# Optimization experiments

Measured on AMD Instinct MI355X. Metric: run time of the kernel, lower is better.

The kernel has to match this reference:

```python
import jax, jax.numpy as jnp
import numpy as np

DIM = 1024
HEADS = 16
HEAD_DIM = DIM // HEADS
HIDDEN = int(DIM * 4.0)
EPS = 1e-5


def setup_inputs() -> dict:
    key = jax.random.key(0)
    ks = jax.random.split(key, 16)
    s = 0.02
    inp = {
        'x': jax.random.normal(ks[0], (2, 2048, DIM), dtype=jnp.float32),
        'g1': jnp.ones((DIM,), jnp.float32),
        'b1': jnp.zeros((DIM,), jnp.float32),
        'Wq': jax.random.normal(ks[1], (DIM, DIM)) * s,
        'bq': jnp.zeros((DIM,), jnp.float32),
        'Wk': jax.random.normal(ks[2], (DIM, DIM)) * s,
        'bk': jnp.zeros((DIM,), jnp.float32),
        'Wv': jax.random.normal(ks[3], (DIM, DIM)) * s,
        'bv': jnp.zeros((DIM,), jnp.float32),
        'Wo': jax.random.normal(ks[4], (DIM, DIM)) * s,
        'bo': jnp.zeros((DIM,), jnp.float32),
        'g2': jnp.ones((DIM,), jnp.float32),
        'b2': jnp.zeros((DIM,), jnp.float32),
        'W1': jax.random.normal(ks[5], (DIM, HIDDEN)) * s,
        'bf1': jnp.zeros((HIDDEN,), jnp.float32),
        'W2': jax.random.normal(ks[6], (HIDDEN, DIM)) * s,
        'bf2': jnp.zeros((DIM,), jnp.float32),
    }
    return inp


def _layernorm(x, g, b):
    mu = jnp.mean(x, axis=-1, keepdims=True)
    var = jnp.mean((x - mu) ** 2, axis=-1, keepdims=True)
    return (x - mu) * jax.lax.rsqrt(var + EPS) * g + b


def _block(x, g1, b1, Wq, bq, Wk, bk, Wv, bv, Wo, bo, g2, b2, W1, bf1, W2, bf2):
    B, N, C = x.shape
    h = _layernorm(x, g1, b1)
    # project and split heads: [B, H, N, D]
    q = (h @ Wq + bq).reshape(B, N, HEADS, HEAD_DIM).transpose(0, 2, 1, 3)
    k = (h @ Wk + bk).reshape(B, N, HEADS, HEAD_DIM).transpose(0, 2, 1, 3)
    v = (h @ Wv + bv).reshape(B, N, HEADS, HEAD_DIM).transpose(0, 2, 1, 3)
    scale = HEAD_DIM ** -0.5
    attn = jnp.einsum('bhqd,bhkd->bhqk', q, k) * scale
    attn = jax.nn.softmax(attn, axis=-1)
    o = jnp.einsum('bhqk,bhkd->bhqd', attn, v)
    o = o.transpose(0, 2, 1, 3).reshape(B, N, C)
    x = x + (o @ Wo + bo)
    h = _layernorm(x, g2, b2)
    h = jax.nn.gelu(h @ W1 + bf1, approximate=False)
    x = x + (h @ W2 + bf2)
    return x


def reference(x, g1, b1, Wq, bq, Wk, bk, Wv, bv, Wo, bo, g2, b2, W1, bf1, W2, bf2):
    return _block(x, g1, b1, Wq, bq, Wk, bk, Wv, bv, Wo, bo, g2, b2, W1, bf1, W2, bf2)
```

## Files before the change

### kernel.cpp

```cpp
#include <hip/hip_runtime.h>
#include <hip/hip_bf16.h>
#include <math.h>


typedef unsigned short ushort_t;
typedef short short8 __attribute__((ext_vector_type(8)));
typedef float f32x4 __attribute__((ext_vector_type(4)));

#define TOKENS 4096
#define SEQ    2048
#define DIMC   1024
#define HID    4096

__device__ __forceinline__ float bf2f(ushort_t u) {
    union { float f; unsigned int u; } c; c.u = ((unsigned int)u) << 16; return c.f;
}
__device__ __forceinline__ ushort_t f2bf(float f) {
    union { float f; unsigned int u; } c; c.f = f;
    unsigned int u = c.u;
    unsigned int r = u + 0x7fffu + ((u >> 16) & 1u);
    return (ushort_t)(r >> 16);
}
__device__ __forceinline__ float gelu_f(float x) {
    const float y = 0.79788456080286536f * (x + 0.044715f * x * x * x);
    const float t = __expf(-2.0f * fabsf(y));
    const float th = (1.0f - t) / (1.0f + t);
    return 0.5f * x * (1.0f + copysignf(th, y));
}
__device__ __forceinline__ float load_elem(const void* p, size_t i, int isbf) {
    return isbf ? bf2f(((const ushort_t*)p)[i]) : ((const float*)p)[i];
}

__global__ __launch_bounds__(256) void detect_dtype(
    const ushort_t* __restrict__ x, int* __restrict__ flag)
{
    __shared__ int bad;
    if (threadIdx.x == 0) bad = 0;
    __syncthreads();
    for (int i = threadIdx.x; i < 4096; i += 256) {
        float v = bf2f(x[i]);
        if (!(fabsf(v) <= 1e6f)) bad = 1;
    }
    __syncthreads();
    if (threadIdx.x == 0) { flag[0] = (bad == 0) ? 1 : 0; flag[1] = 1; }
}

__global__ __launch_bounds__(256) void transpose_w_all(
    const void* __restrict__ Wq, const void* __restrict__ Wk,
    const void* __restrict__ Wv, const void* __restrict__ Wo,
    const void* __restrict__ W1, const void* __restrict__ W2,
    ushort_t* __restrict__ wsq, ushort_t* __restrict__ w1t,
    ushort_t* __restrict__ w2t, const int* __restrict__ flag)
{
    __shared__ ushort_t tile[32][33];
    const int isbf = *flag;
    const int id = blockIdx.x;
    const void* in; ushort_t* out; int K, N, bx, by;
    if (id < 4096) {
        const int z = id >> 10, t = id & 1023;
        in = z == 0 ? Wq : (z == 1 ? Wk : (z == 2 ? Wv : Wo));
        out = wsq + (size_t)z * DIMC * DIMC;
        K = DIMC; N = DIMC; bx = t & 31; by = t >> 5;
    } else if (id < 8192) {
        const int t = id - 4096;
        in = W1; out = w1t; K = DIMC; N = HID;
        bx = t & 127; by = t >> 7;
    } else {
        const int t = id - 8192;
        in = W2; out = w2t; K = HID; N = DIMC;
        bx = t & 31; by = t >> 5;
    }
    const int kb = by * 32, nb = bx * 32;
    const int tx = threadIdx.x & 31, ty = threadIdx.x >> 5;
    for (int i = 0; i < 4; i++) {
        int k = kb + ty + i * 8;
        tile[ty + i * 8][tx] = f2bf(load_elem(in, (size_t)k * N + nb + tx, isbf));
    }
    __syncthreads();
    for (int i = 0; i < 4; i++) {
        int n = nb + ty + i * 8;
        out[(size_t)n * K + kb + tx] = tile[tx][ty + i * 8];
    }
}

template<int INMODE>
__global__ __launch_bounds__(256) void ln_kernel(
    const void* __restrict__ in, const void* __restrict__ g,
    const void* __restrict__ b, const int* __restrict__ flag,
    ushort_t* __restrict__ out)
{
    const int isbf = *flag;
    const int t = blockIdx.x;
    const int tid = threadIdx.x;
    const size_t base = (size_t)t * DIMC;
    float v[4];
    for (int i = 0; i < 4; i++) {
        int idx = tid + i * 256;
        v[i] = (INMODE == 1) ? ((const float*)in)[base + idx]
                             : load_elem(in, base + idx, isbf);
    }
    float s  = v[0] + v[1] + v[2] + v[3];
    float s2 = v[0]*v[0] + v[1]*v[1] + v[2]*v[2] + v[3]*v[3];
    for (int off = 1; off < 64; off <<= 1) {
        s  += __shfl_xor(s,  off);
        s2 += __shfl_xor(s2, off);
    }
    __shared__ float red[8];
    const int wave = tid >> 6, lane = tid & 63;
    if (lane == 0) { red[wave] = s; red[wave + 4] = s2; }
    __syncthreads();
    s  = red[0] + red[1] + red[2] + red[3];
    s2 = red[4] + red[5] + red[6] + red[7];
    const float mu  = s * (1.0f / DIMC);
    const float var = s2 * (1.0f / DIMC) - mu * mu;
    const float inv = rsqrtf(fmaxf(var, 0.f) + 1e-5f);
    for (int i = 0; i < 4; i++) {
        int idx = tid + i * 256;
        float o = (v[i] - mu) * inv * load_elem(g, idx, isbf) + load_elem(b, idx, isbf);
        out[base + idx] = f2bf(o);
    }
}

template<int BN, int RES, int ACT, int OUTF>
__global__ __launch_bounds__(256) void gemm_bt(
    const ushort_t* __restrict__ A, const ushort_t* __restrict__ BT,
    const void* __restrict__ bias0, const void* __restrict__ bias1,
    const void* __restrict__ bias2, const void* __restrict__ resid,
    void* __restrict__ out0, void* __restrict__ out1, void* __restrict__ out2,
    int M, int N, int K, int Ksub, const int* __restrict__ flag)
{
    constexpr int BM   = 128;
    constexpr int JF   = BN / 32;
    constexpr int ASEG = BM / 16;
    constexpr int SPW  = (BM + BN) / 64;
    __shared__ __align__(16) ushort_t As[BM][32];
    __shared__ __align__(16) ushort_t Bs[BN][32];
    const int isbf = *flag;
    const int tid = threadIdx.x, lane = tid & 63, wave = tid >> 6;
    const int m0 = blockIdx.y * BM, n0 = blockIdx.x * BN;
    const int wm = (wave & 1) * 64;
    const int wn = (wave >> 1) * (BN / 2);
    const int lm = lane & 15, quad = lane >> 4;

    const void* biasp = bias0;
    void* outp = out0;
    int nout = N;
    int colmask = 0x7fffffff;
    int sel = 0;
    if (OUTF == 3) {
        sel = n0 >> 10;
        biasp = sel == 0 ? bias0 : (sel == 1 ? bias1 : bias2);
        outp  = sel == 0 ? out0  : (sel == 1 ? out1  : out2);
        nout = 1024; colmask = 1023;
    }
    int kbeg = 0;
    if (OUTF == 4) {
        kbeg = blockIdx.z * Ksub;
        outp = blockIdx.z ? out1 : out0;
    }

    f32x4 acc[4][JF];
    for (int i = 0; i < 4; i++)
        for (int j = 0; j < JF; j++)
            acc[i][j] = (f32x4){0.f, 0.f, 0.f, 0.f};

    const int lrow = lane >> 2;
    const int lcol = (lane & 3) * 8;

    for (int k0 = kbeg; k0 < kbeg + Ksub; k0 += 32) {
#pragma unroll
        for (int s = 0; s < SPW; s++) {
            const int seg = wave * SPW + s;
            const ushort_t* gp;
            ushort_t* lp;
            if (seg < ASEG) {
                gp = &A[(size_t)(m0 + seg * 16 + lrow) * K + k0 + lcol];
                lp = &As[seg * 16][0];
            } else {
                gp = &BT[(size_t)(n0 + (seg - ASEG) * 16 + lrow) * K + k0 + lcol];
                lp = &Bs[(seg - ASEG) * 16][0];
            }
            __builtin_amdgcn_global_load_lds(
                (const __attribute__((address_space(1))) unsigned int*)gp,
                (__attribute__((address_space(3))) unsigned int*)lp, 16, 0, 0);
        }
        __syncthreads();
        short8 af[4], bfr[JF];
#pragma unroll
        for (int i = 0; i < 4; i++) af[i] = *(const short8*)&As[wm + i * 16 + lm][quad * 8];
#pragma unroll
        for (int j = 0; j < JF; j++) bfr[j] = *(const short8*)&Bs[wn + j * 16 + lm][quad * 8];
#pragma unroll
        for (int i = 0; i < 4; i++)
#pragma unroll
            for (int j = 0; j < JF; j++)
                acc[i][j] = __builtin_amdgcn_mfma_f32_16x16x32_bf16(af[i], bfr[j], acc[i][j], 0, 0, 0);
        __syncthreads();
    }

    if (OUTF == 3 && sel == 2) {
        for (int j = 0; j < JF; j++) {
            const int colo = (n0 + wn + j * 16 + lm) & 1023;
            const float bv = load_elem(biasp, colo, isbf);
            for (int i = 0; i < 4; i++) {
                const int token = m0 + wm + i * 16 + quad * 4;
                const int bb = token >> 11, ss = token & 2047;
                unsigned int lo = (unsigned int)f2bf(acc[i][j][0] + bv)
                                | ((unsigned int)f2bf(acc[i][j][1] + bv) << 16);
                unsigned int hi = (unsigned int)f2bf(acc[i][j][2] + bv)
                                | ((unsigned int)f2bf(acc[i][j][3] + bv) << 16);
                *(uint2*)&((ushort_t*)outp)[(size_t)((bb << 10) + colo) * SEQ + ss] =
                    make_uint2(lo, hi);
            }
        }
        return;
    }

    for (int j = 0; j < JF; j++) {
        const int col  = n0 + wn + j * 16 + lm;
        const int colo = col & colmask;
        const float bv = (OUTF == 4) ? 0.f : load_elem(biasp, colo, isbf);
        for (int i = 0; i < 4; i++) {
            const int rbase = m0 + wm + i * 16 + quad * 4;
            for (int r = 0; r < 4; r++) {
                const size_t oi = (size_t)(rbase + r) * nout + colo;
                float v2 = acc[i][j][r] + bv;
                if (ACT == 1) v2 = gelu_f(v2);
                if (RES == 1) v2 += load_elem(resid, oi, isbf);
                if (RES == 2) v2 += ((const float*)resid)[oi];
                if (OUTF == 1 || OUTF == 4) { ((float*)outp)[oi] = v2; }
                else if (OUTF == 2) {
                    if (isbf) ((ushort_t*)outp)[oi] = f2bf(v2);
                    else      ((float*)outp)[oi] = v2;
                }
                else                { ((ushort_t*)outp)[oi] = f2bf(v2); }
            }
        }
    }
}

template<int RESRAW, int OUTF32>
__global__ __launch_bounds__(256) void splitk_reduce(
    const float* __restrict__ p0, const float* __restrict__ p1,
    const void* __restrict__ bias, const void* __restrict__ resid,
    void* __restrict__ out, const int* __restrict__ flag)
{
    const int isbf = *flag;
    const size_t i = ((size_t)blockIdx.x * 256 + threadIdx.x) * 4;
    const float4 a = *(const float4*)&p0[i];
    const float4 b = *(const float4*)&p1[i];
    const int col = (int)(i & 1023);
    float v[4] = {a.x + b.x, a.y + b.y, a.z + b.z, a.w + b.w};
    for (int c = 0; c < 4; c++) {
        v[c] += load_elem(bias, col + c, isbf);
        v[c] += RESRAW ? load_elem(resid, i + c, isbf) : ((const float*)resid)[i + c];
    }
    if (OUTF32) {
        *(float4*)&((float*)out)[i] = make_float4(v[0], v[1], v[2], v[3]);
    } else if (isbf) {
        unsigned int lo = (unsigned int)f2bf(v[0]) | ((unsigned int)f2bf(v[1]) << 16);
        unsigned int hi = (unsigned int)f2bf(v[2]) | ((unsigned int)f2bf(v[3]) << 16);
        *(uint2*)&((ushort_t*)out)[i] = make_uint2(lo, hi);
    } else {
        *(float4*)&((float*)out)[i] = make_float4(v[0], v[1], v[2], v[3]);
    }
}

__global__ __launch_bounds__(256) void attn_kernel(
    const ushort_t* __restrict__ q, const ushort_t* __restrict__ k,
    const ushort_t* __restrict__ vt, ushort_t* __restrict__ o)
{
    const int bh = blockIdx.x;
    const int b  = bh >> 4, h = bh & 15;
    const int q0 = blockIdx.y * 128;
    const int tid = threadIdx.x, lane = tid & 63, wave = tid >> 6;
    const int lm = lane & 15, quad = lane >> 4;

    __shared__ ushort_t Qs[128][72];
    __shared__ ushort_t Ks[64][72];
    __shared__ ushort_t Vt[64][72];
    __shared__ ushort_t Ps[4][32][72];

    const size_t base  = ((size_t)b * SEQ) * DIMC + h * 64;
    const size_t vbase = ((size_t)b * DIMC + h * 64) * SEQ;

    {
        const int er0 = (tid * 8) >> 6;
        const int ec0 = (tid * 8) & 63;
        for (int half = 0; half < 4; half++) {
            const int r = er0 + half * 32;
            short8 qq = *(const short8*)&q[base + (size_t)(q0 + r) * DIMC + ec0];
            short8 qs;
            for (int i = 0; i < 8; i++)
                qs[i] = (short)f2bf(bf2f((ushort_t)qq[i]) * 0.18033688011112042f);
            *(short8*)&Qs[r][ec0] = qs;
        }
    }
    __syncthreads();

    short8 qf[2][2];
    for (int qh = 0; qh < 2; qh++)
        for (int ks = 0; ks < 2; ks++)
            qf[qh][ks] = *(const short8*)&Qs[wave * 32 + qh * 16 + lm][quad * 8 + ks * 32];

    short8 onef;
    for (int i = 0; i < 8; i++) onef[i] = (short)0x3F80;

    f32x4 oacc[4][2], lacc[2];
    for (int j = 0; j < 4; j++)
        for (int qh = 0; qh < 2; qh++) oacc[j][qh] = (f32x4){0.f, 0.f, 0.f, 0.f};
    lacc[0] = (f32x4){0.f, 0.f, 0.f, 0.f};
    lacc[1] = (f32x4){0.f, 0.f, 0.f, 0.f};

    const int er = (tid * 8) >> 6;
    const int ec = (tid * 8) & 63;
    const int dd = tid >> 2;
    const int kg = tid & 3;

    short8 kreg0, kreg1, vreg0, vreg1;
    {
        kreg0 = *(const short8*)&k[base + (size_t)(er) * DIMC + ec];
        kreg1 = *(const short8*)&k[base + (size_t)(er + 32) * DIMC + ec];
        const size_t vsrc = vbase + (size_t)dd * SEQ + kg * 16;
        vreg0 = *(const short8*)&vt[vsrc];
        vreg1 = *(const short8*)&vt[vsrc + 8];
    }

    for (int kt = 0; kt < SEQ / 64; kt++) {
        __syncthreads();
        *(short8*)&Ks[er][ec]          = kreg0;
        *(short8*)&Ks[er + 32][ec]     = kreg1;
        *(short8*)&Vt[dd][kg * 16]     = vreg0;
        *(short8*)&Vt[dd][kg * 16 + 8] = vreg1;
        __syncthreads();
        if (kt + 1 < SEQ / 64) {
            const int kn = (kt + 1) * 64;
            kreg0 = *(const short8*)&k[base + (size_t)(kn + er) * DIMC + ec];
            kreg1 = *(const short8*)&k[base + (size_t)(kn + er + 32) * DIMC + ec];
            const size_t vsrc = vbase + (size_t)dd * SEQ + kn + kg * 16;
            vreg0 = *(const short8*)&vt[vsrc];
            vreg1 = *(const short8*)&vt[vsrc + 8];
        }

        f32x4 st[4][2];
        for (int j = 0; j < 4; j++)
            for (int qh = 0; qh < 2; qh++) st[j][qh] = (f32x4){0.f, 0.f, 0.f, 0.f};
        for (int ks = 0; ks < 2; ks++) {
            for (int j = 0; j < 4; j++) {
                short8 kf = *(const short8*)&Ks[j * 16 + lm][quad * 8 + ks * 32];
                for (int qh = 0; qh < 2; qh++)
                    st[j][qh] = __builtin_amdgcn_mfma_f32_16x16x32_bf16(kf, qf[qh][ks], st[j][qh], 0, 0, 0);
            }
        }

        for (int j = 0; j < 4; j++)
            for (int qh = 0; qh < 2; qh++) {
                unsigned int u0 = __float_as_uint(__builtin_amdgcn_exp2f(st[j][qh][0]));
                unsigned int u1 = __float_as_uint(__builtin_amdgcn_exp2f(st[j][qh][1]));
                unsigned int u2 = __float_as_uint(__builtin_amdgcn_exp2f(st[j][qh][2]));
                unsigned int u3 = __float_as_uint(__builtin_amdgcn_exp2f(st[j][qh][3]));
                unsigned int lo = (u1 & 0xffff0000u) | (u0 >> 16);
                unsigned int hi = (u3 & 0xffff0000u) | (u2 >> 16);
                *(uint2*)&Ps[wave][qh * 16 + lm][j * 16 + quad * 4] = make_uint2(lo, hi);
            }

        for (int ks = 0; ks < 2; ks++) {
            for (int qh = 0; qh < 2; qh++) {
                short8 pf = *(const short8*)&Ps[wave][qh * 16 + lm][quad * 8 + ks * 32];
                lacc[qh] = __builtin_amdgcn_mfma_f32_16x16x32_bf16(pf, onef, lacc[qh], 0, 0, 0);
                for (int j = 0; j < 4; j++) {
                    short8 vf = *(const short8*)&Vt[j * 16 + lm][quad * 8 + ks * 32];
                    oacc[j][qh] = __builtin_amdgcn_mfma_f32_16x16x32_bf16(pf, vf, oacc[j][qh], 0, 0, 0);
                }
            }
        }
    }

    float rinv[2][4];
    for (int qh = 0; qh < 2; qh++)
        for (int r = 0; r < 4; r++) rinv[qh][r] = 1.0f / fmaxf(lacc[qh][r], 1e-30f);

    for (int j = 0; j < 4; j++)
        for (int qh = 0; qh < 2; qh++)
            for (int r = 0; r < 4; r++) {
                const int row = q0 + wave * 32 + qh * 16 + quad * 4 + r;
                o[base + (size_t)row * DIMC + j * 16 + lm] = f2bf(oacc[j][qh][r] * rinv[qh][r]);
            }
}

extern "C" void kernel_launch(void* const* d_in, const int* in_sizes, int n_in,
                              void* d_out, int out_size, void* d_ws, size_t ws_size,
                              hipStream_t stream)
{
    const void* x   = d_in[0];
    const void* g1  = d_in[1];
    const void* b1  = d_in[2];
    const void* Wq  = d_in[3];
    const void* bq  = d_in[4];
    const void* Wk  = d_in[5];
    const void* bk  = d_in[6];
    const void* Wv  = d_in[7];
    const void* bv  = d_in[8];
    const void* Wo  = d_in[9];
    const void* bo  = d_in[10];
    const void* g2  = d_in[11];
    const void* b2  = d_in[12];
    const void* W1  = d_in[13];
    const void* bf1 = d_in[14];
    const void* W2  = d_in[15];
    const void* bf2 = d_in[16];

    const size_t SZ_TOKD_BF = (size_t)TOKENS * DIMC * 2;
    const size_t SZ_TOKD_F  = (size_t)TOKENS * DIMC * 4;
    const size_t SZ_W_SQ    = (size_t)DIMC * DIMC * 2;
    const size_t SZ_W_FF    = (size_t)DIMC * HID * 2;
    const size_t SZ_FF1     = (size_t)TOKENS * HID * 2;

    char* ws = (char*)d_ws;
    size_t off = 0;
    int*      flag = (int*)(ws + off);       off += 256;
    ushort_t* h    = (ushort_t*)(ws + off);  off += SZ_TOKD_BF;
    ushort_t* qb   = (ushort_t*)(ws + off);  off += SZ_TOKD_BF;
    ushort_t* kb_  = (ushort_t*)(ws + off);  off += SZ_TOKD_BF;
    ushort_t* ao   = (ushort_t*)(ws + off);  off += SZ_TOKD_BF;
    ushort_t* vtg  = (ushort_t*)(ws + off);  off += SZ_TOKD_BF;
    float*    x1f  = (float*)qb;
    float*    pa   = (float*)qb;
    float*    p0   = (float*)ao;
    ushort_t* wqt  = (ushort_t*)(ws + off);  off += SZ_W_SQ;
    ushort_t* wkt  = (ushort_t*)(ws + off);  off += SZ_W_SQ;
    ushort_t* wvt  = (ushort_t*)(ws + off);  off += SZ_W_SQ;
    ushort_t* wot  = (ushort_t*)(ws + off);  off += SZ_W_SQ;
    ushort_t* w1t  = (ushort_t*)(ws + off);  off += SZ_W_FF;
    ushort_t* w2t  = (ushort_t*)(ws + off);  off += SZ_W_FF;
    ushort_t* ff1  = (ushort_t*)(ws + off);  off += SZ_FF1;
    float*    p1   = (float*)(ws + off);     off += SZ_TOKD_F;
    if (ws_size < off) return;

    (void)wkt; (void)wvt;

    detect_dtype<<<1, 256, 0, stream>>>((const ushort_t*)x, flag);

    transpose_w_all<<<12288, 256, 0, stream>>>(Wq, Wk, Wv, Wo, W1, W2,
                                               wqt, w1t, w2t, flag);

    ln_kernel<0><<<TOKENS, 256, 0, stream>>>(x, g1, b1, flag, h);

    gemm_bt<64, 0, 0, 3><<<dim3(48, 32), 256, 0, stream>>>(
        h, wqt, bq, bk, bv, nullptr, qb, kb_, vtg, TOKENS, 3072, DIMC, DIMC, flag);

    attn_kernel<<<dim3(32, 16), 256, 0, stream>>>(qb, kb_, vtg, ao);

    gemm_bt<64, 0, 0, 4><<<dim3(16, 32, 2), 256, 0, stream>>>(
        ao, wot, nullptr, nullptr, nullptr, nullptr, pa, p1, nullptr,
        TOKENS, DIMC, DIMC, DIMC / 2, flag);

    splitk_reduce<1, 1><<<TOKENS * DIMC / 1024, 256, 0, stream>>>(
        pa, p1, bo, x, x1f, flag);

    ln_kernel<1><<<TOKENS, 256, 0, stream>>>(x1f, g2, b2, flag, h);

    gemm_bt<64, 0, 1, 0><<<dim3(64, 32), 256, 0, stream>>>(
        h, w1t, bf1, nullptr, nullptr, nullptr, ff1, nullptr, nullptr,
        TOKENS, HID, DIMC, DIMC, flag);

    gemm_bt<64, 0, 0, 4><<<dim3(16, 32, 2), 256, 0, stream>>>(
        ff1, w2t, nullptr, nullptr, nullptr, nullptr, p0, p1, nullptr,
        TOKENS, DIMC, HID, HID / 2, flag);

    splitk_reduce<0, 0><<<TOKENS * DIMC / 1024, 256, 0, stream>>>(
        p0, p1, bf2, x1f, d_out, flag);
}
```

Before: 423.5 us.

## Double-buffer LDS tiles in GEMM to overlap global loads with MFMA

The GEMM main loop now uses two LDS buffers for the A and B tiles. The next K-slice is issued with global_load_lds while MFMAs run on the current buffer, which removes one barrier per step and hides memory latency. Per-thread global and LDS pointers are precomputed once outside the loop. LDS use doubles, which may lower occupancy. The loop assumes the number of K tiles is even.

```diff
diff --git a/kernel.cpp b/kernel.cpp
--- a/kernel.cpp
+++ b/kernel.cpp
@@ -133,8 +133,8 @@
     constexpr int JF   = BN / 32;
     constexpr int ASEG = BM / 16;
     constexpr int SPW  = (BM + BN) / 64;
-    __shared__ __align__(16) ushort_t As[BM][32];
-    __shared__ __align__(16) ushort_t Bs[BN][32];
+    __shared__ __align__(16) ushort_t As[2][BM][32];
+    __shared__ __align__(16) ushort_t Bs[2][BN][32];
     const int isbf = *flag;
     const int tid = threadIdx.x, lane = tid & 63, wave = tid >> 6;
     const int m0 = blockIdx.y * BM, n0 = blockIdx.x * BN;
@@ -167,36 +167,63 @@
     const int lrow = lane >> 2;
     const int lcol = (lane & 3) * 8;
 
-    for (int k0 = kbeg; k0 < kbeg + Ksub; k0 += 32) {
+    const ushort_t* gpp[SPW];
+    ushort_t* lpp[2][SPW];
 #pragma unroll
-        for (int s = 0; s < SPW; s++) {
-            const int seg = wave * SPW + s;
-            const ushort_t* gp;
-            ushort_t* lp;
-            if (seg < ASEG) {
-                gp = &A[(size_t)(m0 + seg * 16 + lrow) * K + k0 + lcol];
-                lp = &As[seg * 16][0];
-            } else {
-                gp = &BT[(size_t)(n0 + (seg - ASEG) * 16 + lrow) * K + k0 + lcol];
-                lp = &Bs[(seg - ASEG) * 16][0];
-            }
-            __builtin_amdgcn_global_load_lds(
-                (const __attribute__((address_space(1))) unsigned int*)gp,
-                (__attribute__((address_space(3))) unsigned int*)lp, 16, 0, 0);
-        }
+    for (int s = 0; s < SPW; s++) {
+        const int seg = wave * SPW + s;
+        if (seg < ASEG) {
+            gpp[s]    = &A[(size_t)(m0 + seg * 16 + lrow) * K + kbeg + lcol];
+            lpp[0][s] = &As[0][seg * 16][0];
+            lpp[1][s] = &As[1][seg * 16][0];
+        } else {
+            gpp[s]    = &BT[(size_t)(n0 + (seg - ASEG) * 16 + lrow) * K + kbeg + lcol];
+            lpp[0][s] = &Bs[0][(seg - ASEG) * 16][0];
+            lpp[1][s] = &Bs[1][(seg - ASEG) * 16][0];
+        }
+    }
+
+#define GEMM_STAGE(BUF, T)                                                    \
+    {                                                                         \
+        _Pragma("unroll")                                                     \
+        for (int s = 0; s < SPW; s++)                                         \
+            __builtin_amdgcn_global_load_lds(                                 \
+                (const __attribute__((address_space(1))) unsigned int*)       \
+                    (gpp[s] + (size_t)(T) * 32),                              \
+                (__attribute__((address_space(3))) unsigned int*)lpp[BUF][s], \
+                16, 0, 0);                                                    \
+    }
+
+#define GEMM_COMPUTE(BUF)                                                     \
+    {                                                                         \
+        short8 af[4], bfr[JF];                                                \
+        _Pragma("unroll")                                                     \
+        for (int i = 0; i < 4; i++)                                           \
+            af[i] = *(const short8*)&As[BUF][wm + i * 16 + lm][quad * 8];     \
+        _Pragma("unroll")                                                     \
+        for (int j = 0; j < JF; j++)                                          \
+            bfr[j] = *(const short8*)&Bs[BUF][wn + j * 16 + lm][quad * 8];    \
+        _Pragma("unroll")                                                     \
+        for (int i = 0; i < 4; i++)                                           \
+            _Pragma("unroll")                                                 \
+            for (int j = 0; j < JF; j++)                                      \
+                acc[i][j] = __builtin_amdgcn_mfma_f32_16x16x32_bf16(          \
+                    af[i], bfr[j], acc[i][j], 0, 0, 0);                       \
+    }
+
+    const int nt = Ksub / 32;
+    GEMM_STAGE(0, 0);
+    __syncthreads();
+    for (int t = 0; t < nt; t += 2) {
+        GEMM_STAGE(1, t + 1);
+        GEMM_COMPUTE(0);
         __syncthreads();
-        short8 af[4], bfr[JF];
-#pragma unroll
-        for (int i = 0; i < 4; i++) af[i] = *(const short8*)&As[wm + i * 16 + lm][quad * 8];
-#pragma unroll
-        for (int j = 0; j < JF; j++) bfr[j] = *(const short8*)&Bs[wn + j * 16 + lm][quad * 8];
-#pragma unroll
-        for (int i = 0; i < 4; i++)
-#pragma unroll
-            for (int j = 0; j < JF; j++)
-                acc[i][j] = __builtin_amdgcn_mfma_f32_16x16x32_bf16(af[i], bfr[j], acc[i][j], 0, 0, 0);
+        if (t + 2 < nt) GEMM_STAGE(0, t + 2);
+        GEMM_COMPUTE(1);
         __syncthreads();
     }
+#undef GEMM_STAGE
+#undef GEMM_COMPUTE
 
     if (OUTF == 3 && sel == 2) {
         for (int j = 0; j < JF; j++) {
```

New measurement: 412.7 us. 1.03x faster.
